# Kernel tuning notes

Hardware: AMD Instinct MI355X
Metric: run time of the kernel (lower is better)

## Reference

```python
import jax, jax.numpy as jnp
import numpy as np

B, T, HID = 4, 2048, 1024
H, FD, HD = 16, 16, 64          # heads, feature_dim, head_dim
CHUNK = 64                      # chunk size for chunked linear attention
EPS_LN = 1e-5                   # layer-norm eps inside feature map
EPS_Z = 1e-10                   # normalize_output eps


def setup_inputs() -> dict:
    key = jax.random.key(0)
    ks = jax.random.split(key, 7)
    init = lambda k, shp: jax.random.normal(k, shp, jnp.float32) * (shp[-1] ** -0.5)
    return {
        "hidden_states": jax.random.normal(ks[0], (B, T, HID), jnp.float32),
        "Wq": init(ks[1], (H * FD, HID)),     # q_proj weight [out,in], no bias
        "Wk": init(ks[2], (H * FD, HID)),
        "Wv": init(ks[3], (H * HD, HID)),
        "Wo": init(ks[4], (H * HD, HID)),
        "gamma": jnp.ones((FD,), jnp.float32),  # RebasedFeatureMap layer-norm scale
        "beta": jnp.zeros((FD,), jnp.float32),  # RebasedFeatureMap layer-norm shift
    }


def _feature_map(x, gamma, beta):
    # layer_norm over feature_dim, then quadratic (outer-product) feature map.
    mu = x.mean(-1, keepdims=True)
    var = ((x - mu) ** 2).mean(-1, keepdims=True)
    xn = (x - mu) * jax.lax.rsqrt(var + EPS_LN) * gamma + beta
    d = xn.shape[-1]
    # [B,T,H,d] -> [B,T,H,d*d]
    x2 = (xn[..., :, None] * xn[..., None, :]).reshape(*xn.shape[:-1], d * d)
    return x2 * (d ** -0.5)


def _chunk_linear_attn(q, k, v):
    # Chunk-recurrent causal linear attention (simple GLA with no gates, scale=1).
    Bq, Tq, Hq, Kq = q.shape
    Vd = v.shape[-1]
    N = Tq // CHUNK
    # [B,T,H,D] -> [N,B,H,C,D] for scan over chunks
    to_chunks = lambda x: x.reshape(Bq, N, CHUNK, Hq, x.shape[-1]).transpose(1, 0, 3, 2, 4)
    qc, kc, vc = to_chunks(q), to_chunks(k), to_chunks(v)
    mask = jnp.tril(jnp.ones((CHUNK, CHUNK), bool))

    def step(state, xs):
        qb, kb, vb = xs  # [B,H,C,K], [B,H,C,K], [B,H,C,V]
        att = jnp.einsum('bhik,bhjk->bhij', qb, kb)
        att = jnp.where(mask, att, 0.0)
        o = jnp.einsum('bhij,bhjv->bhiv', att, vb) + jnp.einsum('bhik,bhkv->bhiv', qb, state)
        state = state + jnp.einsum('bhck,bhcv->bhkv', kb, vb)
        return state, o

    state0 = jnp.zeros((Bq, Hq, Kq, Vd), q.dtype)
    _, o = jax.lax.scan(step, state0, (qc, kc, vc))  # o: [N,B,H,C,V]
    o = o.transpose(1, 0, 3, 2, 4).reshape(Bq, Tq, Hq, Vd)
    # normalize_output: z_t = q_t . cumsum_{s<=t} k_s
    z = jnp.einsum('bthk,bthk->bth', q, jnp.cumsum(k, axis=1))[..., None]
    return o / (z + EPS_Z)


def reference(hidden_states, Wq, Wk, Wv, Wo, gamma, beta):
    Bh, Th, _ = hidden_states.shape
    q = (hidden_states @ Wq.T).reshape(Bh, Th, H, FD)
    k = (hidden_states @ Wk.T).reshape(Bh, Th, H, FD)
    v = (hidden_states @ Wv.T).reshape(Bh, Th, H, HD)
    qf = _feature_map(q, gamma, beta)  # [B,T,H,FD*FD]
    kf = _feature_map(k, gamma, beta)
    o = _chunk_linear_attn(qf, kf, v)  # [B,T,H,HD]
    o = o.reshape(Bh, Th, H * HD)
    return o @ Wo.T
```

## Files before the change

kernel.cpp:

```cpp
#include <hip/hip_runtime.h>

#define T_SEQ 2048
#define BATCH 4
#define NH 16
#define FDIM 16
#define HDIM 64
#define HIDDEN 1024
#define TOK (BATCH * T_SEQ)
#define CH 128
#define NCHUNK (T_SEQ / CH)
#define NBH (BATCH * NH)

#define QK_OFF   0u
#define VT_OFF   4194304u
#define SRAW_OFF 8388608u
#define SPRE_OFF 16777216u
#define MK_OFF   25165824u
#define OAB_OFF  25427968u
#define WQKV_OFF 29622272u
#define WO_OFF   30408704u
#define HSB_OFF  30932992u

typedef float f32x4 __attribute__((ext_vector_type(4)));
typedef short bf16x8 __attribute__((ext_vector_type(8)));
typedef unsigned short us8 __attribute__((ext_vector_type(8)));
typedef unsigned short us4 __attribute__((ext_vector_type(4)));
typedef unsigned int u32;

__device__ __forceinline__ unsigned short f2b(float f) {
  union { float f; unsigned u; } v; v.f = f;
  unsigned r = (v.u + 0x7FFFu + ((v.u >> 16) & 1u)) >> 16;
  return (unsigned short)r;
}
__device__ __forceinline__ float b2f(unsigned short h) {
  union { unsigned u; float f; } v; v.u = ((unsigned)h) << 16; return v.f;
}

__device__ __forceinline__ void gload_lds16(const void* g, void* l) {
  __builtin_amdgcn_global_load_lds(
      (const __attribute__((address_space(1))) u32*)g,
      (__attribute__((address_space(3))) u32*)l, 16, 0, 0);
}

__global__ __launch_bounds__(256) void conv_all(const float* __restrict__ hs,
                                                const float* __restrict__ Wq,
                                                const float* __restrict__ Wk,
                                                const float* __restrict__ Wv,
                                                const float* __restrict__ Wo,
                                                unsigned short* __restrict__ HSB,
                                                unsigned short* __restrict__ WQKVB,
                                                unsigned short* __restrict__ WOB) {
  int i = blockIdx.x * 256 + threadIdx.x;
  const float* src;
  unsigned short* dst;
  if (i < 1048576) {
    int f = i * 8; src = hs + f; dst = HSB + f;
  } else if (i < 1245184) {
    int f = (i - 1048576) * 8;
    if (f < 262144)      src = Wq + f;
    else if (f < 524288) src = Wk + (f - 262144);
    else                 src = Wv + (f - 524288);
    dst = WQKVB + f;
  } else {
    int f = (i - 1245184) * 8;
    src = Wo + f; dst = WOB + f;
  }
  float4 v0 = *(const float4*)src, v1 = *(const float4*)(src + 4);
  us8 o;
  o[0] = f2b(v0.x); o[1] = f2b(v0.y); o[2] = f2b(v0.z); o[3] = f2b(v0.w);
  o[4] = f2b(v1.x); o[5] = f2b(v1.y); o[6] = f2b(v1.z); o[7] = f2b(v1.w);
  *(us8*)dst = o;
}

#define LDSA(p) (lds + (p) * 8192)
#define LDSB(p) (lds + 16384 + (p) * 8192)

__device__ __forceinline__ void stage8(const unsigned short* __restrict__ A,
                                       const unsigned short* __restrict__ B,
                                       int m0, int n0, int kt,
                                       unsigned short* lA, unsigned short* lB,
                                       int w, int lrow, int kswz) {
  const int kc = kt * 64 + kswz;
#pragma unroll
  for (int i = 0; i < 4; ++i) {
    int r = w * 32 + i * 8;
    gload_lds16(&A[(size_t)(m0 + r + lrow) * HIDDEN + kc], &lA[r * 64]);
  }
#pragma unroll
  for (int i = 0; i < 4; ++i) {
    int r = w * 32 + i * 8;
    gload_lds16(&B[(size_t)(n0 + r + lrow) * HIDDEN + kc], &lB[r * 64]);
  }
}

#define RD_A(fm, kk) (*(const bf16x8*)&cA[(wm * 64 + (fm) * 16 + ln) * 64 + (((kk) * 32 + lg * 8) ^ swz)])
#define RD_B(fn, kk) (*(const bf16x8*)&cB[(wn * 64 + (fn) * 16 + ln) * 64 + (((kk) * 32 + lg * 8) ^ swz)])

#define GEMM_PIPELINE(Aptr, Bptr)                                              \
  const int tid = threadIdx.x;                                                 \
  const int lane = tid & 63, w = tid >> 6;                                     \
  const int wm = w >> 1, wn = w & 1;                                           \
  const int ln = lane & 15, lg = lane >> 4;                                    \
  const int lrow = lane >> 3;                                                  \
  const int kswz = (((lane & 7) ^ ((lane >> 3) & 7)) * 8);                     \
  const int swz = (ln & 7) << 3;                                               \
  f32x4 acc[4][4];                                                             \
  _Pragma("unroll") for (int m = 0; m < 4; ++m)                                \
    _Pragma("unroll") for (int n = 0; n < 4; ++n)                              \
      acc[m][n] = (f32x4){0.f, 0.f, 0.f, 0.f};                                 \
  stage8(Aptr, Bptr, m0, n0, 0, LDSA(0), LDSB(0), w, lrow, kswz);              \
  stage8(Aptr, Bptr, m0, n0, 1, LDSA(1), LDSB(1), w, lrow, kswz);              \
  asm volatile("s_waitcnt vmcnt(8)" ::: "memory");                             \
  __builtin_amdgcn_s_barrier();                                                \
  _Pragma("unroll 1") for (int t = 0; t < 16; ++t) {                           \
    const unsigned short* cA = LDSA(t & 1);                                    \
    const unsigned short* cB = LDSB(t & 1);                                    \
    bf16x8 af[4][2], bfr[4][2];                                                \
    _Pragma("unroll") for (int f = 0; f < 4; ++f) {                            \
      af[f][0] = RD_A(f, 0); af[f][1] = RD_A(f, 1);                            \
      bfr[f][0] = RD_B(f, 0); bfr[f][1] = RD_B(f, 1);                          \
    }                                                                          \
    asm volatile("s_waitcnt lgkmcnt(0)" ::: "memory");                         \
    __builtin_amdgcn_sched_barrier(0);                                         \
    __builtin_amdgcn_s_barrier();                                              \
    if (t <= 13)                                                               \
      stage8(Aptr, Bptr, m0, n0, t + 2, LDSA(t & 1), LDSB(t & 1), w, lrow, kswz); \
    __builtin_amdgcn_s_setprio(1);                                             \
    _Pragma("unroll") for (int kk = 0; kk < 2; ++kk)                           \
      _Pragma("unroll") for (int fm = 0; fm < 4; ++fm)                         \
        _Pragma("unroll") for (int fn = 0; fn < 4; ++fn)                       \
          acc[fm][fn] = __builtin_amdgcn_mfma_f32_16x16x32_bf16(               \
              af[fm][kk], bfr[fn][kk], acc[fm][fn], 0, 0, 0);                  \
    __builtin_amdgcn_s_setprio(0);                                             \
    if (t <= 13) { asm volatile("s_waitcnt vmcnt(8)" ::: "memory"); }          \
    else if (t == 14) { asm volatile("s_waitcnt vmcnt(0)" ::: "memory"); }     \
    __builtin_amdgcn_s_barrier();                                              \
  }

__global__ __launch_bounds__(256) void proj_gemm(const unsigned short* __restrict__ A,
                                                 const unsigned short* __restrict__ Wb,
                                                 float* __restrict__ QK,
                                                 unsigned short* __restrict__ VTg) {
  __shared__ unsigned short lds[32768];
  const int bid = blockIdx.x;
  const int logical = (bid & 7) * 96 + (bid >> 3);
  const int bx = logical / 12, by = logical % 12;
  const int m0 = bx * 128, n0 = by * 128;

  GEMM_PIPELINE(A, Wb)

  if (by < 4) {
#pragma unroll
    for (int fm = 0; fm < 4; ++fm)
#pragma unroll
      for (int fn = 0; fn < 4; ++fn) {
        int col = n0 + wn * 64 + fn * 16 + ln;
        int row0 = m0 + wm * 64 + fm * 16 + lg * 4;
#pragma unroll
        for (int j = 0; j < 4; ++j)
          QK[(size_t)(row0 + j) * 512 + col] = acc[fm][fn][j];
      }
  } else {
    unsigned short (*ct)[136] = (unsigned short(*)[136])lds;
#pragma unroll
    for (int fm = 0; fm < 4; ++fm)
#pragma unroll
      for (int fn = 0; fn < 4; ++fn) {
        int cl = wn * 64 + fn * 16 + ln;
        int r0 = wm * 64 + fm * 16 + lg * 4;
        us4 p;
#pragma unroll
        for (int j = 0; j < 4; ++j) p[j] = f2b(acc[fm][fn][j]);
        *(us4*)&ct[cl][r0] = p;
      }
    __builtin_amdgcn_s_barrier();
    asm volatile("" ::: "memory");
    const int vbase = n0 - 512;
    const int b = m0 >> 11, t0 = m0 & 2047;
#pragma unroll
    for (int it = 0; it < 8; ++it) {
      int sid = it * 256 + tid, vl = sid >> 4, tc = sid & 15;
      int vg = vbase + vl, h = vg >> 6, vd = vg & 63;
      us8 val = *(const us8*)&ct[vl][tc * 8];
      *(us8*)&VTg[(((size_t)(b * 16 + h) * 64 + vd) << 11) + t0 + tc * 8] = val;
    }
  }
}

__global__ __launch_bounds__(256) void out_gemm(const unsigned short* __restrict__ A,
                                                const unsigned short* __restrict__ W,
                                                float* __restrict__ C) {
  __shared__ unsigned short lds[32768];
  const int bid = blockIdx.x;
  const int logical = (bid & 7) * 64 + (bid >> 3);
  const int bx = logical >> 3, by = logical & 7;
  const int m0 = bx * 128, n0 = by * 128;

  GEMM_PIPELINE(A, W)

#pragma unroll
  for (int fm = 0; fm < 4; ++fm)
#pragma unroll
    for (int fn = 0; fn < 4; ++fn) {
      int col = n0 + wn * 64 + fn * 16 + ln;
      int row0 = m0 + wm * 64 + fm * 16 + lg * 4;
#pragma unroll
      for (int j = 0; j < 4; ++j)
        C[(size_t)(row0 + j) * 1024 + col] = acc[fm][fn][j];
    }
}

__device__ __forceinline__ void ln16(const float* __restrict__ src,
                                     const float* __restrict__ gamma,
                                     const float* __restrict__ beta,
                                     float* dst) {
  float x[16];
#pragma unroll
  for (int q = 0; q < 4; ++q) {
    float4 v = *(const float4*)(src + q * 4);
    x[q * 4 + 0] = v.x; x[q * 4 + 1] = v.y;
    x[q * 4 + 2] = v.z; x[q * 4 + 3] = v.w;
  }
  float mu = 0.f;
#pragma unroll
  for (int f = 0; f < 16; ++f) mu += x[f];
  mu *= 0.0625f;
  float var = 0.f;
#pragma unroll
  for (int f = 0; f < 16; ++f) { float d = x[f] - mu; var += d * d; }
  var *= 0.0625f;
  const float rs = rsqrtf(var + 1e-5f);
#pragma unroll
  for (int f = 0; f < 16; ++f) dst[f] = (x[f] - mu) * rs * gamma[f] + beta[f];
}

__global__ __launch_bounds__(256) void k_states(const float* __restrict__ QK,
                                                const unsigned short* __restrict__ VTg,
                                                const float* __restrict__ gamma,
                                                const float* __restrict__ beta,
                                                unsigned short* __restrict__ Sraw,
                                                float* __restrict__ Mk) {
  const int c = blockIdx.x, bh = blockIdx.y;
  const int b = bh >> 4, h = bh & 15;
  __shared__ float XKT[16][140];
  __shared__ unsigned short VT[64][152];
  const int tid = threadIdx.x;
  const int lane = tid & 63, wid = tid >> 6;
  const int ln = lane & 15, lg = lane >> 4;

  if (tid < 128) {
    float xr[16];
    ln16(QK + (size_t)(b * T_SEQ + c * CH + tid) * 512 + 256 + h * FDIM, gamma, beta, xr);
#pragma unroll
    for (int f = 0; f < 16; ++f) XKT[f][tid] = xr[f];
  }
#pragma unroll
  for (int it = 0; it < 4; ++it) {
    int flat = tid + it * 256; int v = flat >> 4, sb = flat & 15;
    *(us8*)&VT[v][sb * 8] = *(const us8*)&VTg[((size_t)bh * 64 + v) * T_SEQ + c * CH + sb * 8];
  }
  __syncthreads();

  {
    int i = tid >> 4, j = tid & 15;
    float m = 0.f;
    for (int cc = 0; cc < CH; ++cc) m += XKT[i][cc] * XKT[j][cc];
    Mk[((size_t)bh * NCHUNK + c) * 256 + tid] = m;
  }

  f32x4 acc[4][4];
#pragma unroll
  for (int m = 0; m < 4; ++m)
#pragma unroll
    for (int n = 0; n < 4; ++n) acc[m][n] = (f32x4){0.f, 0.f, 0.f, 0.f};

#pragma unroll
  for (int kt = 0; kt < 4; ++kt) {
    const int s0 = kt * 32 + lg * 8;
    bf16x8 bfr[4];
#pragma unroll
    for (int nt = 0; nt < 4; ++nt) bfr[nt] = *(const bf16x8*)&VT[nt * 16 + ln][s0];
#pragma unroll
    for (int mi = 0; mi < 4; ++mi) {
      const int iidx = wid * 4 + mi;
      float4 xi0 = *(const float4*)&XKT[iidx][s0];
      float4 xi1 = *(const float4*)&XKT[iidx][s0 + 4];
      float4 xj0 = *(const float4*)&XKT[ln][s0];
      float4 xj1 = *(const float4*)&XKT[ln][s0 + 4];
      bf16x8 afr;
      afr[0] = (short)f2b(xi0.x * xj0.x); afr[1] = (short)f2b(xi0.y * xj0.y);
      afr[2] = (short)f2b(xi0.z * xj0.z); afr[3] = (short)f2b(xi0.w * xj0.w);
      afr[4] = (short)f2b(xi1.x * xj1.x); afr[5] = (short)f2b(xi1.y * xj1.y);
      afr[6] = (short)f2b(xi1.z * xj1.z); afr[7] = (short)f2b(xi1.w * xj1.w);
#pragma unroll
      for (int nt = 0; nt < 4; ++nt)
        acc[mi][nt] = __builtin_amdgcn_mfma_f32_16x16x32_bf16(afr, bfr[nt], acc[mi][nt], 0, 0, 0);
    }
  }

  unsigned short* Sp = Sraw + ((size_t)bh * NCHUNK + c) * (64 * 256);
#pragma unroll
  for (int mi = 0; mi < 4; ++mi) {
    int r0 = (wid * 4 + mi) * 16 + lg * 4;
#pragma unroll
    for (int nt = 0; nt < 4; ++nt) {
      int n = nt * 16 + ln;
      us4 pk;
#pragma unroll
      for (int j = 0; j < 4; ++j) pk[j] = f2b(acc[mi][nt][j]);
      *(us4*)&Sp[(size_t)n * 256 + r0] = pk;
    }
  }
}

__global__ __launch_bounds__(256) void k_prefix(const unsigned short* __restrict__ Sraw,
                                                unsigned short* __restrict__ Spre,
                                                float* __restrict__ Mk) {
  const int bh = blockIdx.y;
  if (blockIdx.x < 8) {
    const int e8 = blockIdx.x * 256 + threadIdx.x;
    const int n = (e8 * 8) >> 8, r = (e8 * 8) & 255;
    const int rsw = r ^ ((n & 7) << 3);
    size_t rbase = (size_t)bh * NCHUNK * 16384 + (size_t)e8 * 8;
    size_t wbase = (size_t)bh * NCHUNK * 16384 + (size_t)n * 256 + rsw;
    float run[8] = {0.f, 0.f, 0.f, 0.f, 0.f, 0.f, 0.f, 0.f};
    for (int cc = 0; cc < NCHUNK; ++cc) {
      us8 v = *(const us8*)&Sraw[rbase + (size_t)cc * 16384];
      us8 w;
#pragma unroll
      for (int q = 0; q < 8; ++q) w[q] = f2b(run[q]);
      *(us8*)&Spre[wbase + (size_t)cc * 16384] = w;
#pragma unroll
      for (int q = 0; q < 8; ++q) run[q] += b2f(v[q]);
    }
  } else {
    const int e = threadIdx.x;
    size_t base = (size_t)bh * NCHUNK * 256 + e;
    float run = 0.f;
    for (int c = 0; c < NCHUNK; ++c) {
      float v = Mk[base + (size_t)c * 256];
      Mk[base + (size_t)c * 256] = run;
      run += v;
    }
  }
}

__global__ __launch_bounds__(256) void k_attn_out(const float* __restrict__ QK,
                                                  const unsigned short* __restrict__ VTg,
                                                  const float* __restrict__ gamma,
                                                  const float* __restrict__ beta,
                                                  const unsigned short* __restrict__ Spre,
                                                  const float* __restrict__ Mkp,
                                                  unsigned short* __restrict__ OAB) {
  const int c = blockIdx.x, bh = blockIdx.y;
  const int b = bh >> 4, h = bh & 15;
  __shared__ unsigned short XQb[128][40];
  __shared__ unsigned short XKb[128][40];
  __shared__ unsigned short attb[128 * 128];
  __shared__ unsigned short VT[64][152];
  __shared__ float mksh[256];
  const int tid = threadIdx.x;
  const int lane = tid & 63, wid = tid >> 6;
  const int ln = lane & 15, lg = lane >> 4;

  {
    int r = tid & 127;
    const float* src = QK + (size_t)(b * T_SEQ + c * CH + r) * 512 + (tid < 128 ? 0 : 256) + h * FDIM;
    unsigned short* dst = (tid < 128) ? &XQb[r][0] : &XKb[r][0];
    float xr[16];
    ln16(src, gamma, beta, xr);
    us8 lo, hi, z8;
#pragma unroll
    for (int q = 0; q < 8; ++q) { lo[q] = f2b(xr[q]); hi[q] = f2b(xr[8 + q]); z8[q] = 0; }
    *(us8*)&dst[0] = lo; *(us8*)&dst[8] = hi;
    *(us8*)&dst[16] = z8; *(us8*)&dst[24] = z8;
  }
  {
    const unsigned short* Spg = Spre + ((size_t)bh * NCHUNK + c) * (64 * 256);
#pragma unroll
    for (int it = 0; it < 8; ++it) {
      int seg = it * 4 + wid;
      gload_lds16(&Spg[seg * 512 + lane * 8], &attb[seg * 512]);
    }
  }
#pragma unroll
  for (int it = 0; it < 4; ++it) {
    int flat = tid + it * 256; int v = flat >> 4, sb = flat & 15;
    *(us8*)&VT[v][sb * 8] = *(const us8*)&VTg[((size_t)bh * 64 + v) * T_SEQ + c * CH + sb * 8];
  }
  mksh[tid] = Mkp[((size_t)bh * NCHUNK + c) * 256 + tid];
  __syncthreads();

  const int tb = wid * 32;
  const f32x4 zero4 = {0.f, 0.f, 0.f, 0.f};

  f32x4 o[2][4];
#pragma unroll
  for (int mt = 0; mt < 2; ++mt)
#pragma unroll
    for (int nt = 0; nt < 4; ++nt) o[mt][nt] = zero4;

  {
    bf16x8 xlo0 = *(const bf16x8*)&XQb[tb + ln][0];
    bf16x8 xhi0 = *(const bf16x8*)&XQb[tb + ln][8];
    bf16x8 xlo1 = *(const bf16x8*)&XQb[tb + 16 + ln][0];
    bf16x8 xhi1 = *(const bf16x8*)&XQb[tb + 16 + ln][8];
#pragma unroll
    for (int kt = 0; kt < 8; ++kt) {
      int i = kt * 2 + (lg >> 1);
      float xqi0 = b2f(XQb[tb + ln][i]) * 0.0625f;
      float xqi1 = b2f(XQb[tb + 16 + ln][i]) * 0.0625f;
      bf16x8 sel0 = (lg & 1) ? xhi0 : xlo0;
      bf16x8 sel1 = (lg & 1) ? xhi1 : xlo1;
      bf16x8 qa0, qa1;
#pragma unroll
      for (int jj = 0; jj < 8; ++jj) {
        qa0[jj] = (short)f2b(xqi0 * b2f((unsigned short)sel0[jj]));
        qa1[jj] = (short)f2b(xqi1 * b2f((unsigned short)sel1[jj]));
      }
      int r0 = kt * 32 + lg * 8;
#pragma unroll
      for (int nt = 0; nt < 4; ++nt) {
        int n = nt * 16 + ln;
        bf16x8 bp = *(const bf16x8*)&attb[n * 256 + (r0 ^ ((ln & 7) << 3))];
        o[0][nt] = __builtin_amdgcn_mfma_f32_16x16x32_bf16(qa0, bp, o[0][nt], 0, 0, 0);
        o[1][nt] = __builtin_amdgcn_mfma_f32_16x16x32_bf16(qa1, bp, o[1][nt], 0, 0, 0);
      }
    }
  }

  float zi2[2][4];
#pragma unroll
  for (int mt = 0; mt < 2; ++mt)
#pragma unroll
    for (int j = 0; j < 4; ++j) {
      int t = tb + mt * 16 + lg * 4 + j;
      float xqi = b2f(XQb[t][ln]);
      float p = 0.f;
#pragma unroll
      for (int jm = 0; jm < 16; ++jm) p += b2f(XQb[t][jm]) * mksh[jm * 16 + ln];
      p *= xqi;
      p += __shfl_xor(p, 1, 64);
      p += __shfl_xor(p, 2, 64);
      p += __shfl_xor(p, 4, 64);
      p += __shfl_xor(p, 8, 64);
      zi2[mt][j] = p * 0.0625f;
    }

  __syncthreads();

  bf16x8 aq0 = *(const bf16x8*)&XQb[tb + ln][lg * 8];
  bf16x8 aq1 = *(const bf16x8*)&XQb[tb + 16 + ln][lg * 8];
  float zin[2][4];
#pragma unroll
  for (int mt = 0; mt < 2; ++mt)
#pragma unroll
    for (int j = 0; j < 4; ++j) zin[mt][j] = 0.f;

#pragma unroll
  for (int nt = 0; nt < 8; ++nt) {
    bf16x8 bk = *(const bf16x8*)&XKb[nt * 16 + ln][lg * 8];
    f32x4 c0 = __builtin_amdgcn_mfma_f32_16x16x32_bf16(aq0, bk, zero4, 0, 0, 0);
    f32x4 c1 = __builtin_amdgcn_mfma_f32_16x16x32_bf16(aq1, bk, zero4, 0, 0, 0);
    int s = nt * 16 + ln;
#pragma unroll
    for (int j = 0; j < 4; ++j) {
      int t0 = tb + lg * 4 + j;
      float d0 = c0[j];
      float a0 = (s <= t0) ? d0 * d0 * 0.0625f : 0.f;
      zin[0][j] += a0;
      attb[t0 * 128 + (s ^ ((t0 & 7) << 3))] = f2b(a0);
      int t1 = t0 + 16;
      float d1 = c1[j];
      float a1 = (s <= t1) ? d1 * d1 * 0.0625f : 0.f;
      zin[1][j] += a1;
      attb[t1 * 128 + (s ^ ((t1 & 7) << 3))] = f2b(a1);
    }
  }
#pragma unroll
  for (int mt = 0; mt < 2; ++mt)
#pragma unroll
    for (int j = 0; j < 4; ++j) {
      float zz = zin[mt][j];
      zz += __shfl_xor(zz, 1, 64);
      zz += __shfl_xor(zz, 2, 64);
      zz += __shfl_xor(zz, 4, 64);
      zz += __shfl_xor(zz, 8, 64);
      zin[mt][j] = zz;
    }

#pragma unroll
  for (int kt = 0; kt < 4; ++kt) {
    int s0 = kt * 32 + lg * 8;
    bf16x8 a0 = *(const bf16x8*)&attb[(tb + ln) * 128 + (s0 ^ ((ln & 7) << 3))];
    bf16x8 a1 = *(const bf16x8*)&attb[(tb + 16 + ln) * 128 + (s0 ^ ((ln & 7) << 3))];
#pragma unroll
    for (int nt = 0; nt < 4; ++nt) {
      bf16x8 bv = *(const bf16x8*)&VT[nt * 16 + ln][s0];
      o[0][nt] = __builtin_amdgcn_mfma_f32_16x16x32_bf16(a0, bv, o[0][nt], 0, 0, 0);
      o[1][nt] = __builtin_amdgcn_mfma_f32_16x16x32_bf16(a1, bv, o[1][nt], 0, 0, 0);
    }
  }

  unsigned short* ob = OAB + ((size_t)(b * T_SEQ + c * CH)) * 1024 + h * 64;
#pragma unroll
  for (int mt = 0; mt < 2; ++mt)
#pragma unroll
    for (int j = 0; j < 4; ++j) {
      int t = tb + mt * 16 + lg * 4 + j;
      float inv = 1.0f / (zin[mt][j] + zi2[mt][j] + 1e-10f);
#pragma unroll
      for (int nt = 0; nt < 4; ++nt)
        ob[(size_t)t * 1024 + nt * 16 + ln] = f2b(o[mt][nt][j] * inv);
    }
}

extern "C" void kernel_launch(void* const* d_in, const int* in_sizes, int n_in,
                              void* d_out, int out_size, void* d_ws, size_t ws_size,
                              hipStream_t stream) {
  const float* hs    = (const float*)d_in[0];
  const float* Wq    = (const float*)d_in[1];
  const float* Wk    = (const float*)d_in[2];
  const float* Wv    = (const float*)d_in[3];
  const float* Wo    = (const float*)d_in[4];
  const float* gamma = (const float*)d_in[5];
  const float* beta  = (const float*)d_in[6];
  float* out = (float*)d_out;
  float* ws  = (float*)d_ws;

  float* QK = ws + QK_OFF;
  unsigned short* VTg   = (unsigned short*)(ws + VT_OFF);
  unsigned short* Sraw  = (unsigned short*)(ws + SRAW_OFF);
  unsigned short* Spre  = (unsigned short*)(ws + SPRE_OFF);
  float* Mk = ws + MK_OFF;
  unsigned short* OAB   = (unsigned short*)(ws + OAB_OFF);
  unsigned short* WQKVB = (unsigned short*)(ws + WQKV_OFF);
  unsigned short* WOB   = (unsigned short*)(ws + WO_OFF);
  unsigned short* HSB   = (unsigned short*)(ws + HSB_OFF);

  dim3 blk(256);
  conv_all<<<5376, blk, 0, stream>>>(hs, Wq, Wk, Wv, Wo, HSB, WQKVB, WOB);
  proj_gemm<<<768, blk, 0, stream>>>(HSB, WQKVB, QK, VTg);
  k_states<<<dim3(NCHUNK, NBH), blk, 0, stream>>>(QK, VTg, gamma, beta, Sraw, Mk);
  k_prefix<<<dim3(9, NBH), blk, 0, stream>>>(Sraw, Spre, Mk);
  k_attn_out<<<dim3(NCHUNK, NBH), blk, 0, stream>>>(QK, VTg, gamma, beta, Spre, Mk, OAB);
  out_gemm<<<512, blk, 0, stream>>>(OAB, WOB, out);
}
```

Measured before the change: 125.3 us.

## Store Q/K projections as bf16, compute K Gram matrix with MFMA, prefetch prefix loads

Result: faster. 122.0 us (-2.7%).

```diff
diff --git a/kernel.cpp b/kernel.cpp
--- a/kernel.cpp
+++ b/kernel.cpp
@@ -139,7 +139,7 @@
 
 __global__ __launch_bounds__(256) void proj_gemm(const unsigned short* __restrict__ A,
                                                  const unsigned short* __restrict__ Wb,
-                                                 float* __restrict__ QK,
+                                                 unsigned short* __restrict__ QKB,
                                                  unsigned short* __restrict__ VTg) {
   __shared__ unsigned short lds[32768];
   const int bid = blockIdx.x;
@@ -149,19 +149,26 @@
 
   GEMM_PIPELINE(A, Wb)
 
+  unsigned short (*ct)[136] = (unsigned short(*)[136])lds;
   if (by < 4) {
 #pragma unroll
     for (int fm = 0; fm < 4; ++fm)
 #pragma unroll
       for (int fn = 0; fn < 4; ++fn) {
-        int col = n0 + wn * 64 + fn * 16 + ln;
-        int row0 = m0 + wm * 64 + fm * 16 + lg * 4;
-#pragma unroll
-        for (int j = 0; j < 4; ++j)
-          QK[(size_t)(row0 + j) * 512 + col] = acc[fm][fn][j];
+        int cl = wn * 64 + fn * 16 + ln;
+        int r0 = wm * 64 + fm * 16 + lg * 4;
+#pragma unroll
+        for (int j = 0; j < 4; ++j) ct[r0 + j][cl] = f2b(acc[fm][fn][j]);
       }
+    __builtin_amdgcn_s_barrier();
+    asm volatile("" ::: "memory");
+#pragma unroll
+    for (int it = 0; it < 8; ++it) {
+      int sid = it * 256 + tid, row = sid >> 4, tc = sid & 15;
+      us8 val = *(const us8*)&ct[row][tc * 8];
+      *(us8*)&QKB[(size_t)(m0 + row) * 512 + n0 + tc * 8] = val;
+    }
   } else {
-    unsigned short (*ct)[136] = (unsigned short(*)[136])lds;
 #pragma unroll
     for (int fm = 0; fm < 4; ++fm)
 #pragma unroll
@@ -210,17 +217,15 @@
     }
 }
 
-__device__ __forceinline__ void ln16(const float* __restrict__ src,
-                                     const float* __restrict__ gamma,
-                                     const float* __restrict__ beta,
-                                     float* dst) {
+__device__ __forceinline__ void ln16b(const unsigned short* __restrict__ src,
+                                      const float* __restrict__ gamma,
+                                      const float* __restrict__ beta,
+                                      float* dst) {
+  us8 lo = *(const us8*)src;
+  us8 hi = *(const us8*)(src + 8);
   float x[16];
 #pragma unroll
-  for (int q = 0; q < 4; ++q) {
-    float4 v = *(const float4*)(src + q * 4);
-    x[q * 4 + 0] = v.x; x[q * 4 + 1] = v.y;
-    x[q * 4 + 2] = v.z; x[q * 4 + 3] = v.w;
-  }
+  for (int q = 0; q < 8; ++q) { x[q] = b2f(lo[q]); x[8 + q] = b2f(hi[q]); }
   float mu = 0.f;
 #pragma unroll
   for (int f = 0; f < 16; ++f) mu += x[f];
@@ -234,7 +239,7 @@
   for (int f = 0; f < 16; ++f) dst[f] = (x[f] - mu) * rs * gamma[f] + beta[f];
 }
 
-__global__ __launch_bounds__(256) void k_states(const float* __restrict__ QK,
+__global__ __launch_bounds__(256) void k_states(const unsigned short* __restrict__ QKB,
                                                 const unsigned short* __restrict__ VTg,
                                                 const float* __restrict__ gamma,
                                                 const float* __restrict__ beta,
@@ -250,7 +255,7 @@
 
   if (tid < 128) {
     float xr[16];
-    ln16(QK + (size_t)(b * T_SEQ + c * CH + tid) * 512 + 256 + h * FDIM, gamma, beta, xr);
+    ln16b(QKB + (size_t)(b * T_SEQ + c * CH + tid) * 512 + 256 + h * FDIM, gamma, beta, xr);
 #pragma unroll
     for (int f = 0; f < 16; ++f) XKT[f][tid] = xr[f];
   }
@@ -261,11 +266,23 @@
   }
   __syncthreads();
 
-  {
-    int i = tid >> 4, j = tid & 15;
-    float m = 0.f;
-    for (int cc = 0; cc < CH; ++cc) m += XKT[i][cc] * XKT[j][cc];
-    Mk[((size_t)bh * NCHUNK + c) * 256 + tid] = m;
+  if (wid == 0) {
+    f32x4 g = (f32x4){0.f, 0.f, 0.f, 0.f};
+#pragma unroll
+    for (int kt = 0; kt < 4; ++kt) {
+      const int s0 = kt * 32 + lg * 8;
+      float4 xa = *(const float4*)&XKT[ln][s0];
+      float4 xb = *(const float4*)&XKT[ln][s0 + 4];
+      bf16x8 ga;
+      ga[0] = (short)f2b(xa.x); ga[1] = (short)f2b(xa.y);
+      ga[2] = (short)f2b(xa.z); ga[3] = (short)f2b(xa.w);
+      ga[4] = (short)f2b(xb.x); ga[5] = (short)f2b(xb.y);
+      ga[6] = (short)f2b(xb.z); ga[7] = (short)f2b(xb.w);
+      g = __builtin_amdgcn_mfma_f32_16x16x32_bf16(ga, ga, g, 0, 0, 0);
+    }
+    float* mkp = Mk + ((size_t)bh * NCHUNK + c) * 256;
+#pragma unroll
+    for (int j = 0; j < 4; ++j) mkp[(lg * 4 + j) * 16 + ln] = g[j];
   }
 
   f32x4 acc[4][4];
@@ -324,14 +341,17 @@
     size_t rbase = (size_t)bh * NCHUNK * 16384 + (size_t)e8 * 8;
     size_t wbase = (size_t)bh * NCHUNK * 16384 + (size_t)n * 256 + rsw;
     float run[8] = {0.f, 0.f, 0.f, 0.f, 0.f, 0.f, 0.f, 0.f};
+    us8 v = *(const us8*)&Sraw[rbase];
     for (int cc = 0; cc < NCHUNK; ++cc) {
-      us8 v = *(const us8*)&Sraw[rbase + (size_t)cc * 16384];
-      us8 w;
-#pragma unroll
-      for (int q = 0; q < 8; ++q) w[q] = f2b(run[q]);
-      *(us8*)&Spre[wbase + (size_t)cc * 16384] = w;
+      us8 vn;
+      if (cc < NCHUNK - 1) vn = *(const us8*)&Sraw[rbase + (size_t)(cc + 1) * 16384];
+      us8 wv;
+#pragma unroll
+      for (int q = 0; q < 8; ++q) wv[q] = f2b(run[q]);
+      *(us8*)&Spre[wbase + (size_t)cc * 16384] = wv;
 #pragma unroll
       for (int q = 0; q < 8; ++q) run[q] += b2f(v[q]);
+      v = vn;
     }
   } else {
     const int e = threadIdx.x;
@@ -345,7 +365,7 @@
   }
 }
 
-__global__ __launch_bounds__(256) void k_attn_out(const float* __restrict__ QK,
+__global__ __launch_bounds__(256) void k_attn_out(const unsigned short* __restrict__ QKB,
                                                   const unsigned short* __restrict__ VTg,
                                                   const float* __restrict__ gamma,
                                                   const float* __restrict__ beta,
@@ -365,10 +385,10 @@
 
   {
     int r = tid & 127;
-    const float* src = QK + (size_t)(b * T_SEQ + c * CH + r) * 512 + (tid < 128 ? 0 : 256) + h * FDIM;
+    const unsigned short* src = QKB + (size_t)(b * T_SEQ + c * CH + r) * 512 + (tid < 128 ? 0 : 256) + h * FDIM;
     unsigned short* dst = (tid < 128) ? &XQb[r][0] : &XKb[r][0];
     float xr[16];
-    ln16(src, gamma, beta, xr);
+    ln16b(src, gamma, beta, xr);
     us8 lo, hi, z8;
 #pragma unroll
     for (int q = 0; q < 8; ++q) { lo[q] = f2b(xr[q]); hi[q] = f2b(xr[8 + q]); z8[q] = 0; }
@@ -528,7 +548,7 @@
   float* out = (float*)d_out;
   float* ws  = (float*)d_ws;
 
-  float* QK = ws + QK_OFF;
+  unsigned short* QKB   = (unsigned short*)(ws + QK_OFF);
   unsigned short* VTg   = (unsigned short*)(ws + VT_OFF);
   unsigned short* Sraw  = (unsigned short*)(ws + SRAW_OFF);
   unsigned short* Spre  = (unsigned short*)(ws + SPRE_OFF);
@@ -540,9 +560,9 @@
 
   dim3 blk(256);
   conv_all<<<5376, blk, 0, stream>>>(hs, Wq, Wk, Wv, Wo, HSB, WQKVB, WOB);
-  proj_gemm<<<768, blk, 0, stream>>>(HSB, WQKVB, QK, VTg);
-  k_states<<<dim3(NCHUNK, NBH), blk, 0, stream>>>(QK, VTg, gamma, beta, Sraw, Mk);
+  proj_gemm<<<768, blk, 0, stream>>>(HSB, WQKVB, QKB, VTg);
+  k_states<<<dim3(NCHUNK, NBH), blk, 0, stream>>>(QKB, VTg, gamma, beta, Sraw, Mk);
   k_prefix<<<dim3(9, NBH), blk, 0, stream>>>(Sraw, Spre, Mk);
-  k_attn_out<<<dim3(NCHUNK, NBH), blk, 0, stream>>>(QK, VTg, gamma, beta, Spre, Mk, OAB);
+  k_attn_out<<<dim3(NCHUNK, NBH), blk, 0, stream>>>(QKB, VTg, gamma, beta, Spre, Mk, OAB);
   out_gemm<<<512, blk, 0, stream>>>(OAB, WOB, out);
 }
```
